# Kernel tuning notes

Hardware: AMD Instinct MI355X
Metric: run time of the kernel (lower is better)

## Reference

```python
import jax, jax.numpy as jnp
import numpy as np

G, Q, K, CD, DIM = 2, 8, 1024, 256, 1280
DG = DIM // G
B, N = 8, 4096


def setup_inputs() -> dict:
    key = jax.random.key(0)
    ks = jax.random.split(key, 4)
    rn = lambda k, shape, scale=1.0: jax.random.normal(k, shape, jnp.float32) * scale
    return {
        "x": rn(ks[0], (B, N, DIM)),
        # per-group ResidualVQ input projection: dim/groups -> codebook_dim
        "Win": rn(ks[1], (G, CD, DG), DG ** -0.5),
        "bin": jnp.zeros((G, CD), jnp.float32),
        # per-group output projection: codebook_dim -> dim/groups
        "Wout": rn(ks[2], (G, DG, CD), CD ** -0.5),
        "bout": jnp.zeros((G, DG), jnp.float32),
        # per-group, per-quantizer euclidean codebooks
        "codebooks": rn(ks[3], (G, Q, K, CD)),
    }


def _group_forward(xg, Win, bin_, Wout, bout, cbs):
    h = jnp.einsum('bnd,cd->bnc', xg, Win) + bin_  # project in once (ResidualVQ)

    def step(carry, cb):
        residual, qout = carry
        # squared euclidean distance to every code: (b, n, K)
        d = (jnp.sum(residual * residual, -1, keepdims=True)
             - 2.0 * jnp.einsum('bnc,kc->bnk', residual, cb)
             + jnp.sum(cb * cb, -1))
        idx = jnp.argmin(d, axis=-1)             # (b, n)
        codes = cb[idx]                           # gather (b, n, CD)
        # straight-through estimator
        quantized = residual + jax.lax.stop_gradient(codes - residual)
        # commitment loss (codebook side detached)
        loss = jnp.mean(jnp.square(jax.lax.stop_gradient(quantized) - residual))
        new_res = residual - jax.lax.stop_gradient(quantized)
        return (new_res, qout + quantized), (idx, loss)

    (_, qout), (idxs, losses) = jax.lax.scan(step, (h, jnp.zeros_like(h)), cbs)
    out = jnp.einsum('bnc,dc->bnd', qout, Wout) + bout
    # idxs: (Q, b, n) -> (b, n, Q)
    return out, jnp.moveaxis(idxs, 0, -1), losses


def reference(x, Win, bin, Wout, bout, codebooks):
    b, n, dim = x.shape
    g = Win.shape[0]
    # chunk feature dim into contiguous groups: (g, b, n, dim//g)
    xg = jnp.moveaxis(x.reshape(b, n, g, dim // g), 2, 0)
    out_g, idxs, losses = jax.vmap(_group_forward)(xg, Win, bin, Wout, bout, codebooks)
    quantized = jnp.moveaxis(out_g, 0, 2).reshape(b, n, dim)
    # quantized: (b, n, dim); idxs: (g, b, n, Q); losses: (g, Q)
    return quantized, idxs, losses
```

## Files before the change

kernel.cpp:

```cpp
#include <hip/hip_runtime.h>
#include <hip/hip_bf16.h>


#define G 2
#define Q 8
#define KCODES 1024
#define CD 256
#define DIMV 1280
#define DG 640
#define T 32768
#define TM 128

#define WS_H      ((size_t)0)
#define WS_RES    (WS_H + (size_t)G*T*CD)
#define WS_CNORM  (WS_RES + (size_t)G*T*CD)
#define WS_CN64   (WS_CNORM + (size_t)G*Q*KCODES)
#define WS_LPARTD (WS_CN64 + (size_t)2*G*Q*KCODES)

#define OUT_IDX   ((size_t)T*DIMV)
#define OUT_LOSS  (OUT_IDX + (size_t)G*T*Q)

#define EPS_REFINE 2e-3f
#define ERRB 1e-3

typedef __attribute__((ext_vector_type(8))) short s16x8;
typedef __attribute__((ext_vector_type(4))) float f32x4;

static __device__ __forceinline__ unsigned short f2bf(float v) {
    __hip_bfloat16 b = __float2bfloat16(v);
    return *(unsigned short*)&b;
}
static __device__ __forceinline__ float bf2f(unsigned short u) {
    __hip_bfloat16 b = *(__hip_bfloat16*)&u;
    return __bfloat162float(b);
}

static __device__ __forceinline__ void gl_lds16(const void* g, void* l) {
    __builtin_amdgcn_global_load_lds(
        (const __attribute__((address_space(1))) unsigned int*)g,
        (__attribute__((address_space(3))) unsigned int*)l, 16, 0, 0);
}

__device__ __forceinline__ float np_half_sumsq(const float4* __restrict__ p) {
    float4 a = p[0], b = p[1];
    float r0=a.x*a.x, r1=a.y*a.y, r2=a.z*a.z, r3=a.w*a.w;
    float r4=b.x*b.x, r5=b.y*b.y, r6=b.z*b.z, r7=b.w*b.w;
#pragma unroll
    for (int i = 1; i < 16; i++) {
        a = p[2*i]; b = p[2*i+1];
        r0 += a.x*a.x; r1 += a.y*a.y; r2 += a.z*a.z; r3 += a.w*a.w;
        r4 += b.x*b.x; r5 += b.y*b.y; r6 += b.z*b.z; r7 += b.w*b.w;
    }
    return ((r0+r1)+(r2+r3)) + ((r4+r5)+(r6+r7));
}

__global__ void k_norms(const float* __restrict__ cb, float* __restrict__ ws) {
    int r = blockIdx.x * 256 + threadIdx.x;
    const float4* row = (const float4*)(cb + (size_t)r * CD);
    ws[WS_CNORM + r] = np_half_sumsq(row) + np_half_sumsq(row + 32);
    double s0=0, s1=0, s2=0, s3=0;
#pragma unroll 8
    for (int e = 0; e < 64; e++) {
        float4 v = row[e];
        s0 = fma((double)v.x,(double)v.x,s0); s1 = fma((double)v.y,(double)v.y,s1);
        s2 = fma((double)v.z,(double)v.z,s2); s3 = fma((double)v.w,(double)v.w,s3);
    }
    ((double*)(ws + WS_CN64))[r] = (s0+s1)+(s2+s3);
}

__global__ void k_split(const float* __restrict__ cb, short* __restrict__ cbt) {
    int tau = blockIdx.x * 256 + threadIdx.x;
    int u = tau & 31;
    int row = tau >> 5;
    int gq = row >> 10;
    int code = row & 1023;
    int cc = code >> 5, c32 = code & 31;
    const float* src = cb + (size_t)row * CD + u * 8;
    float4 v0 = *(const float4*)src;
    float4 v1 = *(const float4*)(src + 4);
    float v[8] = {v0.x,v0.y,v0.z,v0.w,v1.x,v1.y,v1.z,v1.w};
    s16x8 hh, ll;
#pragma unroll
    for (int e = 0; e < 8; e++) {
        unsigned short hb = f2bf(v[e]);
        hh[e] = (short)hb;
        ll[e] = (short)f2bf(v[e] - bf2f(hb));
    }
    int n = (u >> 2) * 128 + (u & 3) * 32 + c32;
    size_t base = ((size_t)(gq * 32 + cc) * 2) * 1024;
    *(s16x8*)(cbt + (base + n) * 8)        = hh;
    *(s16x8*)(cbt + (base + 1024 + n) * 8) = ll;
}

__global__ __launch_bounds__(256) void k_proj_in(const float* __restrict__ x,
                                                 const float* __restrict__ Win,
                                                 const float* __restrict__ bin,
                                                 float* __restrict__ ws) {
    __shared__ s16x8 As[780];
    __shared__ s16x8 Bs[780];
    const int g  = blockIdx.z;
    const int t0 = blockIdx.x * 64;
    const int c0 = blockIdx.y * 64;
    const int tid = threadIdx.x;
    const int lane = tid & 63, l15 = lane & 15, l4 = lane >> 4;
    const int wv = tid >> 6, wty = wv >> 1, wtx = wv & 1;
    const int srow = tid >> 2, sku = tid & 3;
    const float* Ag = x + (size_t)g * DG;
    const float* Bg = Win + (size_t)g * CD * DG;
    float* hbuf = ws + WS_H + (size_t)g * T * CD;

    f32x4 acc[2][2];
#pragma unroll
    for (int i = 0; i < 2; i++)
#pragma unroll
        for (int j = 0; j < 2; j++) acc[i][j] = (f32x4){0.f,0.f,0.f,0.f};

    for (int k0 = 0; k0 < DG; k0 += 32) {
        const float* ap = Ag + (size_t)(t0 + srow) * DIMV + k0 + sku * 8;
        const float* bp = Bg + (size_t)(c0 + srow) * DG + k0 + sku * 8;
        float4 a0 = *(const float4*)ap, a1 = *(const float4*)(ap + 4);
        float4 b0 = *(const float4*)bp, b1 = *(const float4*)(bp + 4);
        __syncthreads();
        {
            float va[8] = {a0.x,a0.y,a0.z,a0.w,a1.x,a1.y,a1.z,a1.w};
            float vb[8] = {b0.x,b0.y,b0.z,b0.w,b1.x,b1.y,b1.z,b1.w};
            s16x8 pa[3], pb[3];
#pragma unroll
            for (int e = 0; e < 8; e++) {
                float v = va[e];
                unsigned short q1 = f2bf(v); float r1 = v - bf2f(q1);
                unsigned short q2 = f2bf(r1); float r2 = r1 - bf2f(q2);
                pa[0][e] = (short)q1; pa[1][e] = (short)q2; pa[2][e] = (short)f2bf(r2);
                v = vb[e];
                q1 = f2bf(v); r1 = v - bf2f(q1);
                q2 = f2bf(r1); r2 = r1 - bf2f(q2);
                pb[0][e] = (short)q1; pb[1][e] = (short)q2; pb[2][e] = (short)f2bf(r2);
            }
#pragma unroll
            for (int pl = 0; pl < 3; pl++) {
                As[pl * 260 + sku * 65 + srow] = pa[pl];
                Bs[pl * 260 + sku * 65 + srow] = pb[pl];
            }
        }
        __syncthreads();
#pragma unroll
        for (int ti = 0; ti < 2; ti++) {
            s16x8 aa[3];
#pragma unroll
            for (int pl = 0; pl < 3; pl++)
                aa[pl] = As[pl * 260 + l4 * 65 + wty * 32 + ti * 16 + l15];
#pragma unroll
            for (int tj = 0; tj < 2; tj++) {
                s16x8 bb[3];
#pragma unroll
                for (int pl = 0; pl < 3; pl++)
                    bb[pl] = Bs[pl * 260 + l4 * 65 + wtx * 32 + tj * 16 + l15];
                acc[ti][tj] = __builtin_amdgcn_mfma_f32_16x16x32_bf16(aa[0], bb[0], acc[ti][tj], 0, 0, 0);
                acc[ti][tj] = __builtin_amdgcn_mfma_f32_16x16x32_bf16(aa[0], bb[1], acc[ti][tj], 0, 0, 0);
                acc[ti][tj] = __builtin_amdgcn_mfma_f32_16x16x32_bf16(aa[1], bb[0], acc[ti][tj], 0, 0, 0);
                acc[ti][tj] = __builtin_amdgcn_mfma_f32_16x16x32_bf16(aa[0], bb[2], acc[ti][tj], 0, 0, 0);
                acc[ti][tj] = __builtin_amdgcn_mfma_f32_16x16x32_bf16(aa[2], bb[0], acc[ti][tj], 0, 0, 0);
                acc[ti][tj] = __builtin_amdgcn_mfma_f32_16x16x32_bf16(aa[1], bb[1], acc[ti][tj], 0, 0, 0);
            }
        }
    }
#pragma unroll
    for (int ti = 0; ti < 2; ti++)
#pragma unroll
        for (int tj = 0; tj < 2; tj++) {
            int ccol = c0 + wtx * 32 + tj * 16 + l15;
            float bv = bin[g * CD + ccol];
#pragma unroll
            for (int r = 0; r < 4; r++) {
                int trow = t0 + wty * 32 + ti * 16 + l4 * 4 + r;
                hbuf[(size_t)trow * CD + ccol] = acc[ti][tj][r] + bv;
            }
        }
}

#define STE1F(rv, cv) { float tt_ = __fsub_rn((cv), (rv)); float qq_ = __fadd_rn((rv), tt_); \
                        float rr_ = __fsub_rn((rv), qq_); lacc += (double)rr_ * rr_; (rv) = rr_; }

__global__ __launch_bounds__(256, 2) void k_rvq(const float* __restrict__ cb,
                                                float* __restrict__ ws,
                                                float* __restrict__ out,
                                                const short* __restrict__ cbt) {
    __shared__ s16x8 CbV[2][2048];
    __shared__ float cnS[KCODES];
    __shared__ double lredD[4];

    const int g  = blockIdx.y;
    const int t0 = blockIdx.x * TM;
    const int tid = threadIdx.x;
    const int lane = tid & 63, l15 = lane & 15, l4 = lane >> 4;
    const int wv = tid >> 6;
    const size_t gT = (size_t)g * T;
    const float* cng = ws + WS_CNORM + (size_t)g * Q * KCODES;
    float* hbuf = ws + WS_H;
    float* rbuf = ws + WS_RES;
    double* lpD = (double*)(ws + WS_LPARTD);

    int coff[8];
#pragma unroll
    for (int k = 0; k < 8; k++)
        coff[k] = ((wv * 8 + k) * 64 + lane) * 8;

    s16x8 fh[2][8], fl[2][8];
#pragma unroll
    for (int s = 0; s < 2; s++) {
        const float* hrow = hbuf + (gT + t0 + wv * 32 + s * 16 + l15) * CD + l4 * 8;
#pragma unroll
        for (int dc = 0; dc < 8; dc++) {
            float4 u0 = *(const float4*)(hrow + dc * 32);
            float4 u1 = *(const float4*)(hrow + dc * 32 + 4);
            float v[8] = {u0.x,u0.y,u0.z,u0.w,u1.x,u1.y,u1.z,u1.w};
            s16x8 th, tl;
#pragma unroll
            for (int e = 0; e < 8; e++) {
                unsigned short hb = f2bf(v[e]);
                th[e] = (short)hb;
                tl[e] = (short)f2bf(v[e] - bf2f(hb));
            }
            fh[s][dc] = th; fl[s][dc] = tl;
        }
    }

    for (int q = 0; q < Q; q++) {
        const float* cnq = cng + (size_t)q * KCODES;
        const double* cn64q = (const double*)(ws + WS_CN64) + ((size_t)g * Q + q) * KCODES;
        const float* cqb = cb + ((size_t)g * Q + q) * KCODES * CD;
        const short* cbtq = cbt + (size_t)(g * Q + q) * 524288;
        const float* rsrc = (q == 0) ? hbuf : rbuf;

#pragma unroll
        for (int i = 0; i < 4; i++) cnS[i * 256 + tid] = cnq[i * 256 + tid];

#pragma unroll
        for (int k = 0; k < 8; k++)
            gl_lds16(cbtq + coff[k], &CbV[0][(wv * 8 + k) * 64]);
        __syncthreads();

        float tv1[2] = {3.4e38f, 3.4e38f}, tv2[2] = {3.4e38f, 3.4e38f}, tv3[2] = {3.4e38f, 3.4e38f};
        int   tix[2] = {0x7fffffff, 0x7fffffff}, tix2[2] = {0x7fffffff, 0x7fffffff};
        f32x4 acc[2][2];
#pragma unroll
        for (int s = 0; s < 2; s++)
#pragma unroll
            for (int t = 0; t < 2; t++) acc[s][t] = (f32x4){0.f, 0.f, 0.f, 0.f};

        for (int cc = 0; cc < 32; cc++) {
            __builtin_amdgcn_s_barrier();
            if (cc + 1 < 32) {
                const int add = (cc + 1) * 16384;
#pragma unroll
                for (int k = 0; k < 8; k++)
                    gl_lds16(cbtq + add + coff[k], &CbV[(cc + 1) & 1][(wv * 8 + k) * 64]);
                asm volatile("s_waitcnt vmcnt(8)" ::: "memory");
            } else {
                asm volatile("s_waitcnt vmcnt(0)" ::: "memory");
            }
            __builtin_amdgcn_s_barrier();
            __builtin_amdgcn_sched_barrier(0);

            const int buf = cc & 1;
#pragma unroll
            for (int dc = 0; dc < 8; dc++) {
#pragma unroll
                for (int t = 0; t < 2; t++) {
                    int idx = dc * 128 + l4 * 32 + t * 16 + l15;
                    s16x8 ch = CbV[buf][idx];
                    s16x8 cl2 = CbV[buf][1024 + idx];
#pragma unroll
                    for (int s = 0; s < 2; s++) {
                        acc[s][t] = __builtin_amdgcn_mfma_f32_16x16x32_bf16(ch, fh[s][dc], acc[s][t], 0, 0, 0);
                        acc[s][t] = __builtin_amdgcn_mfma_f32_16x16x32_bf16(ch, fl[s][dc], acc[s][t], 0, 0, 0);
                        acc[s][t] = __builtin_amdgcn_mfma_f32_16x16x32_bf16(cl2, fh[s][dc], acc[s][t], 0, 0, 0);
                    }
                }
            }
#pragma unroll
            for (int s = 0; s < 2; s++)
#pragma unroll
                for (int t = 0; t < 2; t++)
#pragma unroll
                    for (int r = 0; r < 4; r++) {
                        int c = cc * 32 + t * 16 + l4 * 4 + r;
                        float vv = fmaf(-2.f, acc[s][t][r], cnS[c]);
                        if (vv < tv1[s])      { tv3[s] = tv2[s]; tv2[s] = tv1[s]; tix2[s] = tix[s]; tv1[s] = vv; tix[s] = c; }
                        else if (vv < tv2[s]) { tv3[s] = tv2[s]; tv2[s] = vv; tix2[s] = c; }
                        else if (vv < tv3[s]) { tv3[s] = vv; }
                    }
#pragma unroll
            for (int s = 0; s < 2; s++)
#pragma unroll
                for (int t = 0; t < 2; t++) acc[s][t] = (f32x4){0.f, 0.f, 0.f, 0.f};
        }

#pragma unroll
        for (int s = 0; s < 2; s++) {
#pragma unroll
            for (int m = 16; m < 64; m <<= 1) {
                float b1 = __shfl_xor(tv1[s], m, 64);
                int   bi1 = __shfl_xor(tix[s], m, 64);
                float b2 = __shfl_xor(tv2[s], m, 64);
                int   bi2 = __shfl_xor(tix2[s], m, 64);
                float b3 = __shfl_xor(tv3[s], m, 64);
                float n1, n2, n3; int ni1, ni2;
                bool bf = (b1 < tv1[s]) || (b1 == tv1[s] && bi1 < tix[s]);
                if (bf) {
                    n1 = b1; ni1 = bi1;
                    bool af = (tv1[s] < b2) || (tv1[s] == b2 && tix[s] < bi2);
                    if (af) { n2 = tv1[s]; ni2 = tix[s]; n3 = fminf(tv2[s], b2); }
                    else    { n2 = b2;     ni2 = bi2;    n3 = fminf(tv1[s], b3); }
                } else {
                    n1 = tv1[s]; ni1 = tix[s];
                    bool bs = (b1 < tv2[s]) || (b1 == tv2[s] && bi1 < tix2[s]);
                    if (bs) { n2 = b1;     ni2 = bi1;     n3 = fminf(tv2[s], b2); }
                    else    { n2 = tv2[s]; ni2 = tix2[s]; n3 = fminf(b1, tv3[s]); }
                }
                tv1[s] = n1; tix[s] = ni1; tv2[s] = n2; tix2[s] = ni2; tv3[s] = n3;
            }
        }

        int besti[2];
        bool need_full[2];
#pragma unroll 1
        for (int s = 0; s < 2; s++) {
            besti[s] = tix[s];
            need_full[s] = false;
            bool flag = (tv2[s] - tv1[s] < EPS_REFINE);
            if (!__any(flag)) continue;
            const float* rrow = rsrc + (gT + t0 + wv * 32 + s * 16 + l15) * CD + l4 * 8;
            const float* c1r = cqb + (size_t)tix[s]  * CD + l4 * 8;
            const float* c2r = cqb + (size_t)tix2[s] * CD + l4 * 8;
            double d1 = 0.0, d2 = 0.0;
#pragma unroll
            for (int dc = 0; dc < 8; dc++) {
                float4 r0 = *(const float4*)(rrow + dc * 32);
                float4 r1 = *(const float4*)(rrow + dc * 32 + 4);
                float4 p0 = *(const float4*)(c1r + dc * 32);
                float4 p1 = *(const float4*)(c1r + dc * 32 + 4);
                float4 q0 = *(const float4*)(c2r + dc * 32);
                float4 q1 = *(const float4*)(c2r + dc * 32 + 4);
                d1 = fma((double)r0.x,(double)p0.x,d1); d1 = fma((double)r0.y,(double)p0.y,d1);
                d1 = fma((double)r0.z,(double)p0.z,d1); d1 = fma((double)r0.w,(double)p0.w,d1);
                d1 = fma((double)r1.x,(double)p1.x,d1); d1 = fma((double)r1.y,(double)p1.y,d1);
                d1 = fma((double)r1.z,(double)p1.z,d1); d1 = fma((double)r1.w,(double)p1.w,d1);
                d2 = fma((double)r0.x,(double)q0.x,d2); d2 = fma((double)r0.y,(double)q0.y,d2);
                d2 = fma((double)r0.z,(double)q0.z,d2); d2 = fma((double)r0.w,(double)q0.w,d2);
                d2 = fma((double)r1.x,(double)q1.x,d2); d2 = fma((double)r1.y,(double)q1.y,d2);
                d2 = fma((double)r1.z,(double)q1.z,d2); d2 = fma((double)r1.w,(double)q1.w,d2);
            }
#pragma unroll
            for (int m = 16; m < 64; m <<= 1) {
                d1 += __shfl_xor(d1, m, 64);
                d2 += __shfl_xor(d2, m, 64);
            }
            double s1 = fma(-2.0, d1, cn64q[tix[s]]);
            double s2 = fma(-2.0, d2, cn64q[tix2[s]]);
            bool c2wins = (s2 < s1) || (s2 == s1 && tix2[s] < tix[s]);
            double swin = c2wins ? s2 : s1;
            int    iwin = c2wins ? tix2[s] : tix[s];
            if (flag) besti[s] = iwin;
            need_full[s] = flag && !(swin < (double)tv3[s] - ERRB);
        }

#pragma unroll 1
        for (int s = 0; s < 2; s++) {
            unsigned long long flg = __ballot(need_full[s]) & 0xFFFFull;
            while (flg) {
                int l = __builtin_ctzll(flg); flg &= flg - 1;
                const float4* rf4 = (const float4*)(rsrc + (gT + t0 + wv * 32 + s * 16 + l) * CD);
                double bv = 1e300; int bi = 0x7fffffff;
                for (int c = lane; c < KCODES; c += 64) {
                    const float4* cp4 = (const float4*)(cqb + (size_t)c * CD);
                    double a0=0, a1=0, a2=0, a3=0;
#pragma unroll 4
                    for (int e = 0; e < 64; e++) {
                        float4 cv = cp4[e], rv = rf4[e];
                        a0 = fma((double)rv.x,(double)cv.x,a0); a1 = fma((double)rv.y,(double)cv.y,a1);
                        a2 = fma((double)rv.z,(double)cv.z,a2); a3 = fma((double)rv.w,(double)cv.w,a3);
                    }
                    double dd = fma(-2.0, (a0+a1)+(a2+a3), cn64q[c]);
                    if (dd < bv) { bv = dd; bi = c; }
                }
#pragma unroll
                for (int m = 1; m < 64; m <<= 1) {
                    double ov = __shfl_xor(bv, m, 64);
                    int    oi = __shfl_xor(bi, m, 64);
                    if (ov < bv || (ov == bv && oi < bi)) { bv = ov; bi = oi; }
                }
                if (l15 == l) besti[s] = bi;
            }
        }

        if (lane < 16) {
#pragma unroll
            for (int s = 0; s < 2; s++)
                out[OUT_IDX + (gT + t0 + wv * 32 + s * 16 + lane) * Q + q] = (float)besti[s];
        }

        double lacc = 0.0;
#pragma unroll
        for (int s = 0; s < 2; s++) {
            size_t off = (gT + t0 + wv * 32 + s * 16 + l15) * CD + l4 * 8;
            const float* rp = rsrc + off;
            const float* crow = cqb + (size_t)besti[s] * CD + l4 * 8;
            float* wp = rbuf + off;
#pragma unroll
            for (int dc = 0; dc < 8; dc++) {
                float4 r0 = *(const float4*)(rp + dc * 32);
                float4 r1 = *(const float4*)(rp + dc * 32 + 4);
                float4 c0 = *(const float4*)(crow + dc * 32);
                float4 c1 = *(const float4*)(crow + dc * 32 + 4);
                STE1F(r0.x, c0.x); STE1F(r0.y, c0.y); STE1F(r0.z, c0.z); STE1F(r0.w, c0.w);
                STE1F(r1.x, c1.x); STE1F(r1.y, c1.y); STE1F(r1.z, c1.z); STE1F(r1.w, c1.w);
                *(float4*)(wp + dc * 32)     = r0;
                *(float4*)(wp + dc * 32 + 4) = r1;
                float v[8] = {r0.x,r0.y,r0.z,r0.w,r1.x,r1.y,r1.z,r1.w};
                s16x8 th, tl;
#pragma unroll
                for (int e = 0; e < 8; e++) {
                    unsigned short hb = f2bf(v[e]);
                    th[e] = (short)hb;
                    tl[e] = (short)f2bf(v[e] - bf2f(hb));
                }
                fh[s][dc] = th; fl[s][dc] = tl;
            }
        }

#pragma unroll
        for (int m = 1; m < 64; m <<= 1) lacc += __shfl_xor(lacc, m, 64);
        __syncthreads();
        if (lane == 0) lredD[wv] = lacc;
        __syncthreads();
        if (tid == 0)
            lpD[((size_t)g * Q + q) * 256 + blockIdx.x] =
                ((lredD[0] + lredD[1]) + (lredD[2] + lredD[3]));
        __syncthreads();
    }
}

__global__ __launch_bounds__(256) void k_proj_out(const float* __restrict__ ws,
                                                  const float* __restrict__ Wout,
                                                  const float* __restrict__ bout,
                                                  float* __restrict__ out) {
    __shared__ s16x8 As[520];
    __shared__ s16x8 Bs[520];
    const int g  = blockIdx.z;
    const int t0 = blockIdx.x * 64;
    const int d0 = blockIdx.y * 64;
    const int tid = threadIdx.x;
    const int lane = tid & 63, l15 = lane & 15, l4 = lane >> 4;
    const int wv = tid >> 6, wty = wv >> 1, wtx = wv & 1;
    const int srow = tid >> 2, sku = tid & 3;
    const float* Ah = ws + WS_H + (size_t)g * T * CD;
    const float* Ar = ws + WS_RES + (size_t)g * T * CD;
    const float* Bg = Wout + (size_t)g * DG * CD;

    f32x4 acc[2][2];
#pragma unroll
    for (int i = 0; i < 2; i++)
#pragma unroll
        for (int j = 0; j < 2; j++) acc[i][j] = (f32x4){0.f,0.f,0.f,0.f};

    for (int k0 = 0; k0 < CD; k0 += 32) {
        size_t ao = (size_t)(t0 + srow) * CD + k0 + sku * 8;
        const float* bp = Bg + (size_t)(d0 + srow) * CD + k0 + sku * 8;
        float4 h0 = *(const float4*)(Ah + ao), h1 = *(const float4*)(Ah + ao + 4);
        float4 r0 = *(const float4*)(Ar + ao), r1 = *(const float4*)(Ar + ao + 4);
        float4 b0 = *(const float4*)bp, b1 = *(const float4*)(bp + 4);
        __syncthreads();
        {
            float va[8] = {h0.x-r0.x, h0.y-r0.y, h0.z-r0.z, h0.w-r0.w,
                           h1.x-r1.x, h1.y-r1.y, h1.z-r1.z, h1.w-r1.w};
            float vb[8] = {b0.x,b0.y,b0.z,b0.w,b1.x,b1.y,b1.z,b1.w};
            s16x8 pa[2], pb[2];
#pragma unroll
            for (int e = 0; e < 8; e++) {
                float v = va[e];
                unsigned short q1 = f2bf(v);
                pa[0][e] = (short)q1; pa[1][e] = (short)f2bf(v - bf2f(q1));
                v = vb[e];
                q1 = f2bf(v);
                pb[0][e] = (short)q1; pb[1][e] = (short)f2bf(v - bf2f(q1));
            }
#pragma unroll
            for (int pl = 0; pl < 2; pl++) {
                As[pl * 260 + sku * 65 + srow] = pa[pl];
                Bs[pl * 260 + sku * 65 + srow] = pb[pl];
            }
        }
        __syncthreads();
#pragma unroll
        for (int ti = 0; ti < 2; ti++) {
            s16x8 a0f = As[l4 * 65 + wty * 32 + ti * 16 + l15];
            s16x8 a1f = As[260 + l4 * 65 + wty * 32 + ti * 16 + l15];
#pragma unroll
            for (int tj = 0; tj < 2; tj++) {
                s16x8 b0f = Bs[l4 * 65 + wtx * 32 + tj * 16 + l15];
                s16x8 b1f = Bs[260 + l4 * 65 + wtx * 32 + tj * 16 + l15];
                acc[ti][tj] = __builtin_amdgcn_mfma_f32_16x16x32_bf16(a0f, b0f, acc[ti][tj], 0, 0, 0);
                acc[ti][tj] = __builtin_amdgcn_mfma_f32_16x16x32_bf16(a0f, b1f, acc[ti][tj], 0, 0, 0);
                acc[ti][tj] = __builtin_amdgcn_mfma_f32_16x16x32_bf16(a1f, b0f, acc[ti][tj], 0, 0, 0);
            }
        }
    }
#pragma unroll
    for (int ti = 0; ti < 2; ti++)
#pragma unroll
        for (int tj = 0; tj < 2; tj++) {
            int dcol = d0 + wtx * 32 + tj * 16 + l15;
            float bv = bout[g * DG + dcol];
#pragma unroll
            for (int r = 0; r < 4; r++) {
                int trow = t0 + wty * 32 + ti * 16 + l4 * 4 + r;
                out[(size_t)trow * DIMV + (size_t)g * DG + dcol] = acc[ti][tj][r] + bv;
            }
        }
}

__global__ void k_loss(const float* __restrict__ ws, float* __restrict__ out) {
    int gq = blockIdx.x;
    const double* lpD = (const double*)(ws + WS_LPARTD);
    double v = lpD[(size_t)gq * 256 + threadIdx.x];
#pragma unroll
    for (int m = 1; m < 64; m <<= 1) v += __shfl_xor(v, m, 64);
    __shared__ double red[4];
    if ((threadIdx.x & 63) == 0) red[threadIdx.x >> 6] = v;
    __syncthreads();
    if (threadIdx.x == 0)
        out[OUT_LOSS + gq] =
            (float)(((red[0] + red[1]) + (red[2] + red[3])) * (1.0 / 8388608.0));
}

extern "C" void kernel_launch(void* const* d_in, const int* in_sizes, int n_in,
                              void* d_out, int out_size, void* d_ws, size_t ws_size,
                              hipStream_t stream) {
    const float* x    = (const float*)d_in[0];
    const float* Win  = (const float*)d_in[1];
    const float* bin  = (const float*)d_in[2];
    const float* Wout = (const float*)d_in[3];
    const float* bout = (const float*)d_in[4];
    const float* cb   = (const float*)d_in[5];
    float* out = (float*)d_out;
    float* ws  = (float*)d_ws;

    short* cbt = (short*)d_out;

    hipLaunchKernelGGL(k_norms,    dim3(64),          dim3(256), 0, stream, cb, ws);
    hipLaunchKernelGGL(k_split,    dim3(2048),        dim3(256), 0, stream, cb, cbt);
    hipLaunchKernelGGL(k_proj_in,  dim3(T/64, 4, G),  dim3(256), 0, stream, x, Win, bin, ws);
    hipLaunchKernelGGL(k_rvq,      dim3(T/TM, G),     dim3(256), 0, stream, cb, ws, out, cbt);
    hipLaunchKernelGGL(k_proj_out, dim3(T/64, 10, G), dim3(256), 0, stream, ws, Wout, bout, out);
    hipLaunchKernelGGL(k_loss,     dim3(16),          dim3(256), 0, stream, ws, out);
}
```

Before: 1.478 ms.

## Switch codebook staging to 16-code chunks with triple-buffered LDS pipeline

The codebook hi/lo bf16 layout and the RVQ distance loop are reorganized to process 16 codes per chunk instead of 32. LDS is split into three buffers so loads can be issued two chunks ahead, and one of the two barriers per iteration is removed. The aim is deeper prefetch and less sync stall per chunk. In exchange there are twice as many loop iterations, each with less MFMA work, which may leave load latency exposed. The single remaining barrier combined with the vmcnt waits also needs to be enough to protect buffer reuse.

```diff
diff --git a/kernel.cpp b/kernel.cpp
--- a/kernel.cpp
+++ b/kernel.cpp
@@ -74,7 +74,7 @@
     int row = tau >> 5;
     int gq = row >> 10;
     int code = row & 1023;
-    int cc = code >> 5, c32 = code & 31;
+    int cc = code >> 4, c16 = code & 15;
     const float* src = cb + (size_t)row * CD + u * 8;
     float4 v0 = *(const float4*)src;
     float4 v1 = *(const float4*)(src + 4);
@@ -86,10 +86,10 @@
         hh[e] = (short)hb;
         ll[e] = (short)f2bf(v[e] - bf2f(hb));
     }
-    int n = (u >> 2) * 128 + (u & 3) * 32 + c32;
-    size_t base = ((size_t)(gq * 32 + cc) * 2) * 1024;
-    *(s16x8*)(cbt + (base + n) * 8)        = hh;
-    *(s16x8*)(cbt + (base + 1024 + n) * 8) = ll;
+    int n = (u >> 2) * 64 + (u & 3) * 16 + c16;
+    size_t base = (size_t)(gq * 64 + cc) * 1024;
+    *(s16x8*)(cbt + (base + n) * 8)       = hh;
+    *(s16x8*)(cbt + (base + 512 + n) * 8) = ll;
 }
 
 __global__ __launch_bounds__(256) void k_proj_in(const float* __restrict__ x,
@@ -185,7 +185,7 @@
                                                 float* __restrict__ ws,
                                                 float* __restrict__ out,
                                                 const short* __restrict__ cbt) {
-    __shared__ s16x8 CbV[2][2048];
+    __shared__ s16x8 CbV[3][1024];
     __shared__ float cnS[KCODES];
     __shared__ double lredD[4];
 
@@ -200,10 +200,10 @@
     float* rbuf = ws + WS_RES;
     double* lpD = (double*)(ws + WS_LPARTD);
 
-    int coff[8];
-#pragma unroll
-    for (int k = 0; k < 8; k++)
-        coff[k] = ((wv * 8 + k) * 64 + lane) * 8;
+    int coff[4];
+#pragma unroll
+    for (int k = 0; k < 4; k++)
+        coff[k] = ((wv * 4 + k) * 64 + lane) * 8;
 
     s16x8 fh[2][8], fl[2][8];
 #pragma unroll
@@ -236,64 +236,61 @@
         for (int i = 0; i < 4; i++) cnS[i * 256 + tid] = cnq[i * 256 + tid];
 
 #pragma unroll
-        for (int k = 0; k < 8; k++)
-            gl_lds16(cbtq + coff[k], &CbV[0][(wv * 8 + k) * 64]);
+        for (int k = 0; k < 4; k++)
+            gl_lds16(cbtq + coff[k], &CbV[0][(wv * 4 + k) * 64]);
+#pragma unroll
+        for (int k = 0; k < 4; k++)
+            gl_lds16(cbtq + 8192 + coff[k], &CbV[1][(wv * 4 + k) * 64]);
         __syncthreads();
 
         float tv1[2] = {3.4e38f, 3.4e38f}, tv2[2] = {3.4e38f, 3.4e38f}, tv3[2] = {3.4e38f, 3.4e38f};
         int   tix[2] = {0x7fffffff, 0x7fffffff}, tix2[2] = {0x7fffffff, 0x7fffffff};
-        f32x4 acc[2][2];
-#pragma unroll
-        for (int s = 0; s < 2; s++)
-#pragma unroll
-            for (int t = 0; t < 2; t++) acc[s][t] = (f32x4){0.f, 0.f, 0.f, 0.f};
-
-        for (int cc = 0; cc < 32; cc++) {
+        f32x4 acc[2];
+#pragma unroll
+        for (int s = 0; s < 2; s++) acc[s] = (f32x4){0.f, 0.f, 0.f, 0.f};
+
+        int buf = 0;
+        for (int cc = 0; cc < 64; cc++) {
             __builtin_amdgcn_s_barrier();
-            if (cc + 1 < 32) {
-                const int add = (cc + 1) * 16384;
-#pragma unroll
-                for (int k = 0; k < 8; k++)
-                    gl_lds16(cbtq + add + coff[k], &CbV[(cc + 1) & 1][(wv * 8 + k) * 64]);
+            if (cc + 2 < 64) {
+                const int add = (cc + 2) * 8192;
+                const int nb = (buf + 2 >= 3) ? buf - 1 : buf + 2;
+#pragma unroll
+                for (int k = 0; k < 4; k++)
+                    gl_lds16(cbtq + add + coff[k], &CbV[nb][(wv * 4 + k) * 64]);
                 asm volatile("s_waitcnt vmcnt(8)" ::: "memory");
+            } else if (cc + 2 == 64) {
+                asm volatile("s_waitcnt vmcnt(4)" ::: "memory");
             } else {
                 asm volatile("s_waitcnt vmcnt(0)" ::: "memory");
             }
-            __builtin_amdgcn_s_barrier();
             __builtin_amdgcn_sched_barrier(0);
 
-            const int buf = cc & 1;
 #pragma unroll
             for (int dc = 0; dc < 8; dc++) {
-#pragma unroll
-                for (int t = 0; t < 2; t++) {
-                    int idx = dc * 128 + l4 * 32 + t * 16 + l15;
-                    s16x8 ch = CbV[buf][idx];
-                    s16x8 cl2 = CbV[buf][1024 + idx];
-#pragma unroll
-                    for (int s = 0; s < 2; s++) {
-                        acc[s][t] = __builtin_amdgcn_mfma_f32_16x16x32_bf16(ch, fh[s][dc], acc[s][t], 0, 0, 0);
-                        acc[s][t] = __builtin_amdgcn_mfma_f32_16x16x32_bf16(ch, fl[s][dc], acc[s][t], 0, 0, 0);
-                        acc[s][t] = __builtin_amdgcn_mfma_f32_16x16x32_bf16(cl2, fh[s][dc], acc[s][t], 0, 0, 0);
-                    }
+                int idx = dc * 64 + l4 * 16 + l15;
+                s16x8 ch = CbV[buf][idx];
+                s16x8 cl2 = CbV[buf][512 + idx];
+#pragma unroll
+                for (int s = 0; s < 2; s++) {
+                    acc[s] = __builtin_amdgcn_mfma_f32_16x16x32_bf16(ch, fh[s][dc], acc[s], 0, 0, 0);
+                    acc[s] = __builtin_amdgcn_mfma_f32_16x16x32_bf16(ch, fl[s][dc], acc[s], 0, 0, 0);
+                    acc[s] = __builtin_amdgcn_mfma_f32_16x16x32_bf16(cl2, fh[s][dc], acc[s], 0, 0, 0);
                 }
             }
 #pragma unroll
-            for (int s = 0; s < 2; s++)
-#pragma unroll
-                for (int t = 0; t < 2; t++)
-#pragma unroll
-                    for (int r = 0; r < 4; r++) {
-                        int c = cc * 32 + t * 16 + l4 * 4 + r;
-                        float vv = fmaf(-2.f, acc[s][t][r], cnS[c]);
-                        if (vv < tv1[s])      { tv3[s] = tv2[s]; tv2[s] = tv1[s]; tix2[s] = tix[s]; tv1[s] = vv; tix[s] = c; }
-                        else if (vv < tv2[s]) { tv3[s] = tv2[s]; tv2[s] = vv; tix2[s] = c; }
-                        else if (vv < tv3[s]) { tv3[s] = vv; }
-                    }
-#pragma unroll
-            for (int s = 0; s < 2; s++)
-#pragma unroll
-                for (int t = 0; t < 2; t++) acc[s][t] = (f32x4){0.f, 0.f, 0.f, 0.f};
+            for (int s = 0; s < 2; s++) {
+#pragma unroll
+                for (int r = 0; r < 4; r++) {
+                    int c = cc * 16 + l4 * 4 + r;
+                    float vv = fmaf(-2.f, acc[s][r], cnS[c]);
+                    if (vv < tv1[s])      { tv3[s] = tv2[s]; tv2[s] = tv1[s]; tix2[s] = tix[s]; tv1[s] = vv; tix[s] = c; }
+                    else if (vv < tv2[s]) { tv3[s] = tv2[s]; tv2[s] = vv; tix2[s] = c; }
+                    else if (vv < tv3[s]) { tv3[s] = vv; }
+                }
+                acc[s] = (f32x4){0.f, 0.f, 0.f, 0.f};
+            }
+            buf = (buf + 1 >= 3) ? 0 : buf + 1;
         }
 
 #pragma unroll
```

Measured after the change: 1.595 ms. 1.08x slower.
